# Performance work log

Measured on AMD Instinct MI355X. Metric: run time of the kernel, lower is better.

The kernel has to match this reference:

```python
import jax, jax.numpy as jnp
import numpy as np

B, S, H, W = 256, 512, 1024, 64  # batch, seq, hidden_dim, context_window

def setup_inputs() -> dict:
    key = jax.random.key(0)
    k1, k2, k3, k4, k5, k6 = jax.random.split(key, 6)
    inputs = jax.random.normal(k1, (B, S, H), jnp.float32)
    # lengths must be >= context_window and <= S
    setence_len = W + jax.random.randint(k2, (B,), 0, S - W + 1)
    # parent < W <= len ensures len - parent - 1 >= 0 (valid index)
    parent = jax.random.randint(k3, (B,), 0, W)
    hc = jax.random.normal(k4, (B, H), jnp.float32)
    # nn.Linear(2H, H) params
    W_attn = jax.random.normal(k5, (H, 2 * H), jnp.float32) * (1.0 / np.sqrt(2 * H))
    b_attn = jnp.zeros((H,), jnp.float32)
    # nn.Parameter(torch.rand(H)) -> uniform [0,1)
    v = jax.random.uniform(k6, (H,), jnp.float32)
    return {"inputs": inputs, "hc": hc, "W_attn": W_attn, "b_attn": b_attn,
            "v": v, "setence_len": setence_len, "parent": parent}

def reference(inputs, hc, W_attn, b_attn, v, setence_len, parent):
    # Mt: per-sample window inputs[b, len_b-W:len_b, :] -> [B, W, H]
    idx = setence_len[:, None] - W + jnp.arange(W)[None, :]          # [B, W]
    Mt = jnp.take_along_axis(inputs, idx[:, :, None], axis=1)        # [B, W, H]
    # par: inputs[b, len_b - parent_b - 1, :] -> [B, H]
    pidx = (setence_len - parent - 1)[:, None, None]                 # [B, 1, 1]
    par = jnp.take_along_axis(inputs, pidx, axis=1)[:, 0, :]         # [B, H]
    # h = hc repeated over the window axis -> [B, W, H]
    h = jnp.broadcast_to(hc[:, None, :], Mt.shape)
    # additive (Bahdanau) scoring
    energy = jnp.tanh(jnp.concatenate([h, Mt], axis=-1) @ W_attn.T + b_attn)  # [B, W, H]
    scores = jnp.einsum('h,bwh->bw', v, energy)                      # [B, W]
    attn = jax.nn.softmax(scores, axis=-1)                           # [B, W]
    attn_weights = attn[:, None, :]                                  # [B, 1, W]
    context = jnp.einsum('bw,bwh->bh', attn, Mt)[:, None, :]         # [B, 1, H]
    return attn_weights, context, par
```

## Files before the change

kernel.cpp:

```cpp
#include <hip/hip_runtime.h>
#include <math.h>

#define Bdim 256
#define Sdim 512
#define Hdim 1024
#define Wdim 64
#define BK 32
#define JTILE 256
#define NJT 4
#define MTILE 128
#define KC 4

typedef __attribute__((ext_vector_type(8))) short bf16x8;
typedef __attribute__((ext_vector_type(4))) float f32x4;

#define WS_SCORES_F (NJT * Bdim * Wdim)
#define WS_PART_F   (KC * Bdim * Hdim)
#define WS_WSP_F    (Hdim * Hdim / 2)
#define WS_NEED_BYTES  ((size_t)(WS_SCORES_F + WS_PART_F) * 4)
#define WS_MFMA_BYTES  ((size_t)(WS_SCORES_F + WS_PART_F + WS_WSP_F) * 4)

#define ASTRIDE 140
#define AS_F (BK * ASTRIDE)
#define SMEM_F (AS_F + BK * JTILE)
#define HC0_OFF 0
#define HCW_OFF 2048
#define VS_OFF  2560

__device__ __forceinline__ unsigned pk2(unsigned short a, unsigned short b) {
  return (unsigned)a | ((unsigned)b << 16);
}

__global__ __launch_bounds__(256) void k_wsplit(
    const float* __restrict__ Wa, unsigned short* __restrict__ wsp)
{
  const int j = blockIdx.x;
  const int t = threadIdx.x;
  const float4 xv = *(const float4*)(Wa + (size_t)j * (2 * Hdim) + Hdim + 4 * t);
  unsigned short h[4], l[4];
  #pragma unroll
  for (int e = 0; e < 4; ++e) {
    const float x = ((const float*)&xv)[e];
    const unsigned u = __float_as_uint(x);
    const float hif = __uint_as_float(u & 0xFFFF0000u);
    const float lof = x - hif;
    h[e] = (unsigned short)(u >> 16);
    l[e] = (unsigned short)(__float_as_uint(lof) >> 16);
  }
  const int kc = (4 * t) >> 5, ki = (4 * t) & 31;
  unsigned short* base = wsp + (size_t)j * 2048 + kc * 64 + ki;
  *(ushort4*)(base)      = make_ushort4(h[0], h[1], h[2], h[3]);
  *(ushort4*)(base + 32) = make_ushort4(l[0], l[1], l[2], l[3]);
}

__global__ __launch_bounds__(256) void k_hcw(
    const float* __restrict__ hc, const float* __restrict__ Wa,
    float* __restrict__ part)
{
  const int jt = blockIdx.x, bt = blockIdx.y, kc = blockIdx.z;
  const int t = threadIdx.x;
  const int b0 = bt * 16;
  const int kb = kc * 256;
  __shared__ float As[BK][20];
  __shared__ float Bs[BK][256];
  const int tb = t & 3, tj = t >> 2;
  float acc[4][4] = {{0.f}};
  const float* brow = Wa + (size_t)(jt * 256 + t) * (2 * Hdim) + kb;
  const int r = t & 15, kq = t >> 4;
  for (int k0 = 0; k0 < 256; k0 += BK) {
    float4 bld[8];
    #pragma unroll
    for (int q = 0; q < 8; ++q) bld[q] = *(const float4*)(brow + k0 + q * 4);
    float4 ald = make_float4(0.f, 0.f, 0.f, 0.f);
    if (t < 128) ald = *(const float4*)(hc + (size_t)(b0 + r) * Hdim + kb + k0 + kq * 4);
    __syncthreads();
    #pragma unroll
    for (int q = 0; q < 8; ++q)
      #pragma unroll
      for (int e = 0; e < 4; ++e)
        Bs[q * 4 + e][t] = ((const float*)&bld[q])[e];
    if (t < 128) {
      #pragma unroll
      for (int e = 0; e < 4; ++e) As[kq * 4 + e][r] = ((const float*)&ald)[e];
    }
    __syncthreads();
    #pragma unroll 8
    for (int k = 0; k < BK; ++k) {
      const float4 av = *(const float4*)&As[k][tb * 4];
      const float4 bv = *(const float4*)&Bs[k][tj * 4];
      const float A4[4] = {av.x, av.y, av.z, av.w};
      const float B4[4] = {bv.x, bv.y, bv.z, bv.w};
      #pragma unroll
      for (int i = 0; i < 4; ++i)
        #pragma unroll
        for (int jj = 0; jj < 4; ++jj)
          acc[i][jj] = fmaf(A4[i], B4[jj], acc[i][jj]);
    }
  }
  float* outp = part + (size_t)kc * (Bdim * Hdim);
  #pragma unroll
  for (int i = 0; i < 4; ++i)
    #pragma unroll
    for (int jj = 0; jj < 4; ++jj)
      outp[(size_t)(b0 + tb * 4 + i) * Hdim + jt * 256 + tj * 4 + jj] = acc[i][jj];
}

__global__ __launch_bounds__(512) void k_scores_mfma(
    const float* __restrict__ inputs, const float* __restrict__ ba,
    const float* __restrict__ v, const int* __restrict__ slen,
    float* __restrict__ ws_scores, const float* __restrict__ part,
    const unsigned short* __restrict__ wsp)
{
  const int jt = blockIdx.x;
  const int b0 = blockIdx.y * 4;
  const int t = threadIdx.x;
  const int lane = t & 63, wv = t >> 6, wm = wv >> 1, wn = wv & 1;

  __shared__ uint4 lds4[65536 / 16];
  char* As = (char*)lds4;
  char* Bs = (char*)lds4 + 32768;

  const int ar = t >> 1, ah = t & 1;
  const int ab = ar >> 6;
  const int slA = slen[b0 + ab];
  const float* aptr = inputs +
      ((size_t)(b0 + ab) * Sdim + slA - Wdim + (ar & 63)) * Hdim + ah * 16;
  const int arw = ar & 7;
  char* aw0 = As + ar * 128;
  const int bj = t >> 1, bc = t & 1;
  const unsigned short* bptr = wsp + (size_t)(jt * 256 + bj) * 2048 + bc * 32;
  const int bjw = bj & 7;
  char* bw0 = Bs + bj * 128;

  int aoff[4][2], boff[8][2];
  #pragma unroll
  for (int mt = 0; mt < 4; ++mt) {
    const int row = wm * 64 + mt * 16 + (lane & 15);
    const int s0 = lane >> 4;
    aoff[mt][0] = row * 128 + ((s0 ^ (row & 7)) << 4);
    aoff[mt][1] = row * 128 + (((s0 + 4) ^ (row & 7)) << 4);
  }
  #pragma unroll
  for (int nt = 0; nt < 8; ++nt) {
    const int row = wn * 128 + nt * 16 + (lane & 15);
    const int s0 = lane >> 4;
    boff[nt][0] = row * 128 + ((s0 ^ (row & 7)) << 4);
    boff[nt][1] = row * 128 + (((s0 + 4) ^ (row & 7)) << 4);
  }

  f32x4 acc[4][8];
  #pragma unroll
  for (int mt = 0; mt < 4; ++mt)
    #pragma unroll
    for (int nt = 0; nt < 8; ++nt) {
      f32x4 z = {0.f, 0.f, 0.f, 0.f};
      acc[mt][nt] = z;
    }

  float4 a_ld[4];
  uint4  b_ld[4];
  #pragma unroll
  for (int c = 0; c < 4; ++c) a_ld[c] = *(const float4*)(aptr + c * 4);
  #pragma unroll
  for (int q = 0; q < 4; ++q) b_ld[q] = *(const uint4*)(bptr + q * 8);

  for (int k0 = 0; k0 < Hdim; k0 += 32) {
    __syncthreads();
    unsigned short h[16], l[16];
    #pragma unroll
    for (int c = 0; c < 4; ++c)
      #pragma unroll
      for (int e = 0; e < 4; ++e) {
        const float x = ((const float*)&a_ld[c])[e];
        const unsigned u = __float_as_uint(x);
        const float hif = __uint_as_float(u & 0xFFFF0000u);
        const float lof = x - hif;
        h[c * 4 + e] = (unsigned short)(u >> 16);
        l[c * 4 + e] = (unsigned short)(__float_as_uint(lof) >> 16);
      }
    uint4 H0 = make_uint4(pk2(h[0], h[1]), pk2(h[2], h[3]), pk2(h[4], h[5]), pk2(h[6], h[7]));
    uint4 H1 = make_uint4(pk2(h[8], h[9]), pk2(h[10], h[11]), pk2(h[12], h[13]), pk2(h[14], h[15]));
    uint4 L0 = make_uint4(pk2(l[0], l[1]), pk2(l[2], l[3]), pk2(l[4], l[5]), pk2(l[6], l[7]));
    uint4 L1 = make_uint4(pk2(l[8], l[9]), pk2(l[10], l[11]), pk2(l[12], l[13]), pk2(l[14], l[15]));
    *(uint4*)(aw0 + (((2 * ah + 0) ^ arw) << 4)) = H0;
    *(uint4*)(aw0 + (((2 * ah + 1) ^ arw) << 4)) = H1;
    *(uint4*)(aw0 + (((4 + 2 * ah + 0) ^ arw) << 4)) = L0;
    *(uint4*)(aw0 + (((4 + 2 * ah + 1) ^ arw) << 4)) = L1;
    #pragma unroll
    for (int q = 0; q < 4; ++q)
      *(uint4*)(bw0 + (((bc * 4 + q) ^ bjw) << 4)) = b_ld[q];
    if (k0 + 32 < Hdim) {
      #pragma unroll
      for (int c = 0; c < 4; ++c) a_ld[c] = *(const float4*)(aptr + k0 + 32 + c * 4);
      const int kc = (k0 + 32) >> 5;
      #pragma unroll
      for (int q = 0; q < 4; ++q) b_ld[q] = *(const uint4*)(bptr + kc * 64 + q * 8);
    }
    __syncthreads();
    bf16x8 ahf[4], alf[4];
    #pragma unroll
    for (int mt = 0; mt < 4; ++mt) {
      ahf[mt] = *(const bf16x8*)(As + aoff[mt][0]);
      alf[mt] = *(const bf16x8*)(As + aoff[mt][1]);
    }
    #pragma unroll
    for (int nt = 0; nt < 8; ++nt) {
      const bf16x8 bh = *(const bf16x8*)(Bs + boff[nt][0]);
      const bf16x8 bl = *(const bf16x8*)(Bs + boff[nt][1]);
      #pragma unroll
      for (int mt = 0; mt < 4; ++mt) {
        acc[mt][nt] = __builtin_amdgcn_mfma_f32_16x16x32_bf16(ahf[mt], bh, acc[mt][nt], 0, 0, 0);
        acc[mt][nt] = __builtin_amdgcn_mfma_f32_16x16x32_bf16(alf[mt], bh, acc[mt][nt], 0, 0, 0);
        acc[mt][nt] = __builtin_amdgcn_mfma_f32_16x16x32_bf16(ahf[mt], bl, acc[mt][nt], 0, 0, 0);
      }
    }
  }

  __syncthreads();
  float* scr   = (float*)lds4;
  float* hcw_s = scr;
  float* v_s   = scr + 1024;
  float* red   = scr + 1280;
  for (int idx = t; idx < 1024; idx += 512) {
    const int bb = idx >> 8, jj = idx & 255;
    const int jg = jt * 256 + jj;
    float s = ba[jg];
    #pragma unroll
    for (int kc = 0; kc < KC; ++kc)
      s += part[(size_t)kc * (Bdim * Hdim) + (size_t)(b0 + bb) * Hdim + jg];
    hcw_s[idx] = s;
  }
  if (t < 256) v_s[t] = v[jt * 256 + t];
  __syncthreads();

  float sred[4][4];
  #pragma unroll
  for (int mt = 0; mt < 4; ++mt)
    #pragma unroll
    for (int r = 0; r < 4; ++r) sred[mt][r] = 0.f;
  #pragma unroll
  for (int nt = 0; nt < 8; ++nt) {
    const int col = wn * 128 + nt * 16 + (lane & 15);
    const float hw0 = hcw_s[wm * 256 + col];
    const float vj = v_s[col];
    #pragma unroll
    for (int mt = 0; mt < 4; ++mt)
      #pragma unroll
      for (int r = 0; r < 4; ++r) {
        const float s = ((const float*)&acc[mt][nt])[r] + hw0;
        sred[mt][r] = fmaf(vj, tanhf(s), sred[mt][r]);
      }
  }
  #pragma unroll
  for (int mt = 0; mt < 4; ++mt)
    #pragma unroll
    for (int r = 0; r < 4; ++r) {
      float x = sred[mt][r];
      x += __shfl_xor(x, 1); x += __shfl_xor(x, 2);
      x += __shfl_xor(x, 4); x += __shfl_xor(x, 8);
      sred[mt][r] = x;
    }
  if ((lane & 15) == 0) {
    #pragma unroll
    for (int mt = 0; mt < 4; ++mt)
      #pragma unroll
      for (int r = 0; r < 4; ++r)
        red[wn * 256 + wm * 64 + mt * 16 + (lane >> 4) * 4 + r] = sred[mt][r];
  }
  __syncthreads();
  if (t < 256) {
    const float s = red[t] + red[256 + t];
    ws_scores[(size_t)jt * (Bdim * Wdim) + (size_t)(b0 + (t >> 6)) * Wdim + (t & 63)] = s;
  }
}

template<int USE_PART>
__global__ __launch_bounds__(256, 2) void k_scores(
    const float* __restrict__ inputs, const float* __restrict__ hc,
    const float* __restrict__ Wa, const float* __restrict__ ba,
    const float* __restrict__ v, const int* __restrict__ slen,
    float* __restrict__ ws_scores, const float* __restrict__ part)
{
  const int jt = blockIdx.x;
  const int b0 = blockIdx.y * 2;
  const int t = threadIdx.x;
  __shared__ float smem[SMEM_F];
  float* Bsb = smem + AS_F;

  const int tw = t & 15, tj = t >> 4;
  const int w0 = tw * 8, j0 = tj * 16;
  const int awp = w0 + 4 * (tw >> 2);

  const int ar = t >> 1, ah = t & 1;
  const int absub = ar >> 6;
  const int slA = slen[b0 + absub];
  const float* arow = inputs +
      ((size_t)(b0 + absub) * Sdim + slA - Wdim + (ar & 63)) * Hdim + ah * 16;
  const int aphys = ar + 4 * (ar >> 5);
  const float* brow = Wa + (size_t)(jt * JTILE + t) * (2 * Hdim) + Hdim;

  float acc[8][16];
  #pragma unroll
  for (int i = 0; i < 8; ++i)
    #pragma unroll
    for (int jj = 0; jj < 16; ++jj) acc[i][jj] = 0.f;

  for (int k0 = 0; k0 < Hdim; k0 += BK) {
    float4 a_ld[4];
    #pragma unroll
    for (int c = 0; c < 4; ++c) a_ld[c] = *(const float4*)(arow + k0 + c * 4);
    float4 b_ld[8];
    #pragma unroll
    for (int q = 0; q < 8; ++q) b_ld[q] = *(const float4*)(brow + k0 + q * 4);
    __syncthreads();
    #pragma unroll
    for (int c = 0; c < 4; ++c)
      #pragma unroll
      for (int e = 0; e < 4; ++e)
        smem[(ah * 16 + c * 4 + e) * ASTRIDE + aphys] = ((const float*)&a_ld[c])[e];
    #pragma unroll
    for (int q = 0; q < 8; ++q)
      #pragma unroll
      for (int e = 0; e < 4; ++e)
        Bsb[(q * 4 + e) * JTILE + t] = ((const float*)&b_ld[q])[e];
    __syncthreads();
    #pragma unroll 8
    for (int k = 0; k < BK; ++k) {
      const float* Ak = smem + k * ASTRIDE;
      const float* Bk = Bsb + k * JTILE;
      const float4 av0 = *(const float4*)(Ak + awp);
      const float4 av1 = *(const float4*)(Ak + awp + 4);
      const float4 bv0 = *(const float4*)(Bk + j0);
      const float4 bv1 = *(const float4*)(Bk + j0 + 4);
      const float4 bv2 = *(const float4*)(Bk + j0 + 8);
      const float4 bv3 = *(const float4*)(Bk + j0 + 12);
      const float A8[8]  = {av0.x, av0.y, av0.z, av0.w, av1.x, av1.y, av1.z, av1.w};
      const float B16[16] = {bv0.x, bv0.y, bv0.z, bv0.w, bv1.x, bv1.y, bv1.z, bv1.w,
                             bv2.x, bv2.y, bv2.z, bv2.w, bv3.x, bv3.y, bv3.z, bv3.w};
      #pragma unroll
      for (int wi = 0; wi < 8; ++wi)
        #pragma unroll
        for (int ji = 0; ji < 16; ++ji)
          acc[wi][ji] = fmaf(A8[wi], B16[ji], acc[wi][ji]);
    }
  }

  __syncthreads();
  const int j = jt * JTILE + t;
  if (USE_PART) {
    float h0 = ba[j], h1 = ba[j];
    #pragma unroll
    for (int kc = 0; kc < KC; ++kc) {
      h0 += part[(size_t)kc * (Bdim * Hdim) + (size_t)b0 * Hdim + j];
      h1 += part[(size_t)kc * (Bdim * Hdim) + (size_t)(b0 + 1) * Hdim + j];
    }
    smem[HCW_OFF + t] = h0;
    smem[HCW_OFF + 256 + t] = h1;
    smem[VS_OFF + t] = v[j];
  } else {
    for (int i = t; i < 2 * Hdim; i += 256) smem[HC0_OFF + i] = hc[(size_t)b0 * Hdim + i];
    __syncthreads();
    const float* w1row = Wa + (size_t)j * (2 * Hdim);
    float s0 = 0.f, s1 = 0.f;
    #pragma unroll 4
    for (int k = 0; k < Hdim; k += 4) {
      const float4 wv  = *(const float4*)(w1row + k);
      const float4 h0v = *(const float4*)(smem + HC0_OFF + k);
      const float4 h1v = *(const float4*)(smem + HC0_OFF + Hdim + k);
      s0 = fmaf(wv.x, h0v.x, s0); s0 = fmaf(wv.y, h0v.y, s0);
      s0 = fmaf(wv.z, h0v.z, s0); s0 = fmaf(wv.w, h0v.w, s0);
      s1 = fmaf(wv.x, h1v.x, s1); s1 = fmaf(wv.y, h1v.y, s1);
      s1 = fmaf(wv.z, h1v.z, s1); s1 = fmaf(wv.w, h1v.w, s1);
    }
    __syncthreads();
    smem[HCW_OFF + t] = s0 + ba[j];
    smem[HCW_OFF + 256 + t] = s1 + ba[j];
    smem[VS_OFF + t] = v[j];
  }
  __syncthreads();

  const int bsub = tw >> 3;
  float sloc[8] = {0.f, 0.f, 0.f, 0.f, 0.f, 0.f, 0.f, 0.f};
  #pragma unroll
  for (int ji = 0; ji < 16; ++ji) {
    const float hw = smem[HCW_OFF + bsub * 256 + j0 + ji];
    const float vj = smem[VS_OFF + j0 + ji];
    #pragma unroll
    for (int wi = 0; wi < 8; ++wi)
      sloc[wi] = fmaf(vj, tanhf(acc[wi][ji] + hw), sloc[wi]);
  }
  float* red = smem + AS_F;
  #pragma unroll
  for (int wi = 0; wi < 8; ++wi) red[tj * MTILE + w0 + wi] = sloc[wi];
  __syncthreads();
  if (t < MTILE) {
    float s = 0.f;
    #pragma unroll
    for (int p = 0; p < 16; ++p) s += red[p * MTILE + t];
    ws_scores[(size_t)jt * (Bdim * Wdim) + (size_t)(b0 + (t >> 6)) * Wdim + (t & 63)] = s;
  }
}

__global__ __launch_bounds__(256) void k_finish(
    const float* __restrict__ inputs, const int* __restrict__ slen,
    const int* __restrict__ parent, const float* __restrict__ ws_scores,
    float* __restrict__ out)
{
  const int b = blockIdx.x;
  const int c = blockIdx.y;
  const int t = threadIdx.x;
  const int sl = slen[b];
  __shared__ float attn[64];

  if (t < 64) {
    float s = ws_scores[b * Wdim + t]
            + ws_scores[1 * (Bdim * Wdim) + b * Wdim + t]
            + ws_scores[2 * (Bdim * Wdim) + b * Wdim + t]
            + ws_scores[3 * (Bdim * Wdim) + b * Wdim + t];
    float mx = s;
    #pragma unroll
    for (int off = 32; off > 0; off >>= 1) mx = fmaxf(mx, __shfl_xor(mx, off));
    const float e = __expf(s - mx);
    float sm = e;
    #pragma unroll
    for (int off = 32; off > 0; off >>= 1) sm += __shfl_xor(sm, off);
    const float a = e / sm;
    if (c == 0) out[b * Wdim + t] = a;
    attn[t] = a;
  }
  __syncthreads();

  const float* base = inputs + ((size_t)b * Sdim + sl - Wdim) * Hdim + c * 256;
  float a0 = 0.f;
  #pragma unroll 8
  for (int w = 0; w < Wdim; ++w)
    a0 = fmaf(attn[w], base[(size_t)w * Hdim + t], a0);
  out[Bdim * Wdim + (size_t)b * Hdim + c * 256 + t] = a0;

  const float* pr = inputs + ((size_t)b * Sdim + sl - parent[b] - 1) * Hdim + c * 256;
  out[Bdim * Wdim + Bdim * Hdim + (size_t)b * Hdim + c * 256 + t] = pr[t];
}

extern "C" void kernel_launch(void* const* d_in, const int* in_sizes, int n_in,
                              void* d_out, int out_size, void* d_ws, size_t ws_size,
                              hipStream_t stream) {
  const float* inputs = (const float*)d_in[0];
  const float* hc     = (const float*)d_in[1];
  const float* Wa     = (const float*)d_in[2];
  const float* ba     = (const float*)d_in[3];
  const float* v      = (const float*)d_in[4];
  const int*   slen   = (const int*)d_in[5];
  const int*   parent = (const int*)d_in[6];
  float* out = (float*)d_out;
  float* ws  = (float*)d_ws;
  float* part = ws + WS_SCORES_F;
  unsigned short* wsp = (unsigned short*)(ws + WS_SCORES_F + WS_PART_F);

  if (ws_size >= WS_MFMA_BYTES) {
    k_wsplit<<<dim3(Hdim), 256, 0, stream>>>(Wa, wsp);
    k_hcw<<<dim3(NJT, 16, KC), 256, 0, stream>>>(hc, Wa, part);
    k_scores_mfma<<<dim3(NJT, Bdim / 4), 512, 0, stream>>>(
        inputs, ba, v, slen, ws, part, wsp);
  } else if (ws_size >= WS_NEED_BYTES) {
    k_hcw<<<dim3(NJT, 16, KC), 256, 0, stream>>>(hc, Wa, part);
    k_scores<1><<<dim3(NJT, Bdim / 2), 256, 0, stream>>>(
        inputs, hc, Wa, ba, v, slen, ws, part);
  } else {
    k_scores<0><<<dim3(NJT, Bdim / 2), 256, 0, stream>>>(
        inputs, hc, Wa, ba, v, slen, ws, nullptr);
  }
  k_finish<<<dim3(Bdim, 4), 256, 0, stream>>>(inputs, slen, parent, ws, out);
}
```

Before: 818.2 us.

## Pre-split activations into swizzled bf16 hi/lo and stream via global_load_lds

Adds a prep kernel that gathers each sample's window rows and splits them into bf16 hi/lo pairs. These are stored in global memory already in the swizzled LDS tile layout, and the weight split kernel now writes the same layout. The scores kernel then copies tiles directly into LDS with global_load_lds instead of converting in registers. It also halves the N tile to 128 columns, doubles the grid along N, and raises occupancy via launch bounds. The aim is to remove per-iteration conversion and packing work from the MFMA loop. The costs are a large extra workspace buffer, an extra pass that writes it out, activation data re-read by twice as many N tiles, and an unpipelined load-then-wait per K step.

```diff
diff --git a/kernel.cpp b/kernel.cpp
--- a/kernel.cpp
+++ b/kernel.cpp
@@ -10,15 +10,17 @@
 #define NJT 4
 #define MTILE 128
 #define KC 4
+#define NJT2 8
 
 typedef __attribute__((ext_vector_type(8))) short bf16x8;
 typedef __attribute__((ext_vector_type(4))) float f32x4;
 
-#define WS_SCORES_F (NJT * Bdim * Wdim)
+#define WS_SCORES_F (NJT2 * Bdim * Wdim)
 #define WS_PART_F   (KC * Bdim * Hdim)
 #define WS_WSP_F    (Hdim * Hdim / 2)
-#define WS_NEED_BYTES  ((size_t)(WS_SCORES_F + WS_PART_F) * 4)
-#define WS_MFMA_BYTES  ((size_t)(WS_SCORES_F + WS_PART_F + WS_WSP_F) * 4)
+#define WS_APRE_F   (Bdim * Wdim * Hdim)
+#define WS_NEED_BYTES   ((size_t)(WS_SCORES_F + WS_PART_F) * 4)
+#define WS_MFMA_BYTES   ((size_t)(WS_SCORES_F + WS_PART_F + WS_WSP_F + WS_APRE_F) * 4)
 
 #define ASTRIDE 140
 #define AS_F (BK * ASTRIDE)
@@ -27,8 +29,21 @@
 #define HCW_OFF 2048
 #define VS_OFF  2560
 
-__device__ __forceinline__ unsigned pk2(unsigned short a, unsigned short b) {
-  return (unsigned)a | ((unsigned)b << 16);
+#if defined(__has_builtin)
+#if __has_builtin(__builtin_amdgcn_global_load_lds)
+#define HAS_GLL 1
+#endif
+#endif
+#ifndef HAS_GLL
+#define HAS_GLL 0
+#endif
+
+__device__ __forceinline__ void gll16(const void* g, void* l) {
+#if HAS_GLL
+  __builtin_amdgcn_global_load_lds(
+      (const __attribute__((address_space(1))) void*)g,
+      (__attribute__((address_space(3))) void*)l, 16, 0, 0);
+#endif
 }
 
 __global__ __launch_bounds__(256) void k_wsplit(
@@ -36,6 +51,7 @@
 {
   const int j = blockIdx.x;
   const int t = threadIdx.x;
+  const int jt = j >> 7, jr = j & 127;
   const float4 xv = *(const float4*)(Wa + (size_t)j * (2 * Hdim) + Hdim + 4 * t);
   unsigned short h[4], l[4];
   #pragma unroll
@@ -43,14 +59,42 @@
     const float x = ((const float*)&xv)[e];
     const unsigned u = __float_as_uint(x);
     const float hif = __uint_as_float(u & 0xFFFF0000u);
-    const float lof = x - hif;
     h[e] = (unsigned short)(u >> 16);
-    l[e] = (unsigned short)(__float_as_uint(lof) >> 16);
-  }
-  const int kc = (4 * t) >> 5, ki = (4 * t) & 31;
-  unsigned short* base = wsp + (size_t)j * 2048 + kc * 64 + ki;
-  *(ushort4*)(base)      = make_ushort4(h[0], h[1], h[2], h[3]);
-  *(ushort4*)(base + 32) = make_ushort4(l[0], l[1], l[2], l[3]);
+    l[e] = (unsigned short)(__float_as_uint(x - hif) >> 16);
+  }
+  const int kc = t >> 3;
+  const int ls = (t >> 1) & 3;
+  const int sw = jr & 7;
+  char* base = (char*)wsp + (((size_t)(jt * 32 + kc) * 128 + jr) << 7) + (t & 1) * 8;
+  *(ushort4*)(base + ((ls ^ sw) << 4))       = make_ushort4(h[0], h[1], h[2], h[3]);
+  *(ushort4*)(base + (((ls + 4) ^ sw) << 4)) = make_ushort4(l[0], l[1], l[2], l[3]);
+}
+
+__global__ __launch_bounds__(256) void k_aprep(
+    const float* __restrict__ inputs, const int* __restrict__ slen,
+    unsigned short* __restrict__ apre)
+{
+  const int w = blockIdx.x, b = blockIdx.y;
+  const int t = threadIdx.x;
+  const int gr = b * 64 + w;
+  const int r = gr & 255, bg = gr >> 8;
+  const int sl = slen[b];
+  const float4 xv = *(const float4*)(inputs + ((size_t)b * Sdim + sl - Wdim + w) * Hdim + 4 * t);
+  unsigned short h[4], l[4];
+  #pragma unroll
+  for (int e = 0; e < 4; ++e) {
+    const float x = ((const float*)&xv)[e];
+    const unsigned u = __float_as_uint(x);
+    const float hif = __uint_as_float(u & 0xFFFF0000u);
+    h[e] = (unsigned short)(u >> 16);
+    l[e] = (unsigned short)(__float_as_uint(x - hif) >> 16);
+  }
+  const int kc = t >> 3;
+  const int ls = (t >> 1) & 3;
+  const int sw = r & 7;
+  char* base = (char*)apre + (((size_t)(bg * 32 + kc) * 256 + r) << 7) + (t & 1) * 8;
+  *(ushort4*)(base + ((ls ^ sw) << 4))       = make_ushort4(h[0], h[1], h[2], h[3]);
+  *(ushort4*)(base + (((ls + 4) ^ sw) << 4)) = make_ushort4(l[0], l[1], l[2], l[3]);
 }
 
 __global__ __launch_bounds__(256) void k_hcw(
@@ -105,132 +149,105 @@
       outp[(size_t)(b0 + tb * 4 + i) * Hdim + jt * 256 + tj * 4 + jj] = acc[i][jj];
 }
 
-__global__ __launch_bounds__(512) void k_scores_mfma(
-    const float* __restrict__ inputs, const float* __restrict__ ba,
-    const float* __restrict__ v, const int* __restrict__ slen,
-    float* __restrict__ ws_scores, const float* __restrict__ part,
-    const unsigned short* __restrict__ wsp)
+__global__ __launch_bounds__(512, 4) void k_scores_mfma2(
+    const unsigned short* __restrict__ apre, const unsigned short* __restrict__ wsp,
+    const float* __restrict__ ba, const float* __restrict__ v,
+    float* __restrict__ ws_scores, const float* __restrict__ part)
 {
   const int jt = blockIdx.x;
-  const int b0 = blockIdx.y * 4;
-  const int t = threadIdx.x;
-  const int lane = t & 63, wv = t >> 6, wm = wv >> 1, wn = wv & 1;
-
-  __shared__ uint4 lds4[65536 / 16];
-  char* As = (char*)lds4;
-  char* Bs = (char*)lds4 + 32768;
-
-  const int ar = t >> 1, ah = t & 1;
-  const int ab = ar >> 6;
-  const int slA = slen[b0 + ab];
-  const float* aptr = inputs +
-      ((size_t)(b0 + ab) * Sdim + slA - Wdim + (ar & 63)) * Hdim + ah * 16;
-  const int arw = ar & 7;
-  char* aw0 = As + ar * 128;
-  const int bj = t >> 1, bc = t & 1;
-  const unsigned short* bptr = wsp + (size_t)(jt * 256 + bj) * 2048 + bc * 32;
-  const int bjw = bj & 7;
-  char* bw0 = Bs + bj * 128;
-
-  int aoff[4][2], boff[8][2];
+  const int bg = blockIdx.y;
+  const int t = threadIdx.x;
+  const int lane = t & 63, wv = t >> 6;
+  const int wm = wv >> 1, wn = wv & 1;
+
+  __shared__ uint4 ldsv[49152 / 16];
+  char* lds = (char*)ldsv;
+
+  const int s0 = lane >> 4;
+  int aoff[4][2], boff[4][2];
   #pragma unroll
   for (int mt = 0; mt < 4; ++mt) {
     const int row = wm * 64 + mt * 16 + (lane & 15);
-    const int s0 = lane >> 4;
     aoff[mt][0] = row * 128 + ((s0 ^ (row & 7)) << 4);
     aoff[mt][1] = row * 128 + (((s0 + 4) ^ (row & 7)) << 4);
   }
   #pragma unroll
-  for (int nt = 0; nt < 8; ++nt) {
-    const int row = wn * 128 + nt * 16 + (lane & 15);
-    const int s0 = lane >> 4;
-    boff[nt][0] = row * 128 + ((s0 ^ (row & 7)) << 4);
-    boff[nt][1] = row * 128 + (((s0 + 4) ^ (row & 7)) << 4);
-  }
-
-  f32x4 acc[4][8];
+  for (int nt = 0; nt < 4; ++nt) {
+    const int row = wn * 64 + nt * 16 + (lane & 15);
+    boff[nt][0] = 32768 + row * 128 + ((s0 ^ (row & 7)) << 4);
+    boff[nt][1] = 32768 + row * 128 + (((s0 + 4) ^ (row & 7)) << 4);
+  }
+
+  f32x4 acc[4][4];
   #pragma unroll
   for (int mt = 0; mt < 4; ++mt)
     #pragma unroll
-    for (int nt = 0; nt < 8; ++nt) {
+    for (int nt = 0; nt < 4; ++nt) {
       f32x4 z = {0.f, 0.f, 0.f, 0.f};
       acc[mt][nt] = z;
     }
 
-  float4 a_ld[4];
-  uint4  b_ld[4];
-  #pragma unroll
-  for (int c = 0; c < 4; ++c) a_ld[c] = *(const float4*)(aptr + c * 4);
-  #pragma unroll
-  for (int q = 0; q < 4; ++q) b_ld[q] = *(const uint4*)(bptr + q * 8);
-
-  for (int k0 = 0; k0 < Hdim; k0 += 32) {
-    __syncthreads();
-    unsigned short h[16], l[16];
-    #pragma unroll
-    for (int c = 0; c < 4; ++c)
-      #pragma unroll
-      for (int e = 0; e < 4; ++e) {
-        const float x = ((const float*)&a_ld[c])[e];
-        const unsigned u = __float_as_uint(x);
-        const float hif = __uint_as_float(u & 0xFFFF0000u);
-        const float lof = x - hif;
-        h[c * 4 + e] = (unsigned short)(u >> 16);
-        l[c * 4 + e] = (unsigned short)(__float_as_uint(lof) >> 16);
+  const char* aB = (const char*)apre + ((size_t)bg << 20) + wv * 4096 + (lane << 4);
+  const char* bB = (const char*)wsp + ((size_t)jt << 19) + wv * 2048 + (lane << 4);
+  char* aL = lds + wv * 4096;
+  char* bL = lds + 32768 + wv * 2048;
+
+  for (int kc = 0; kc < 32; ++kc) {
+    __syncthreads();
+    const char* ac = aB + ((size_t)kc << 15);
+    const char* bc = bB + ((size_t)kc << 14);
+#if HAS_GLL
+    gll16(ac,        aL);
+    gll16(ac + 1024, aL + 1024);
+    gll16(ac + 2048, aL + 2048);
+    gll16(ac + 3072, aL + 3072);
+    gll16(bc,        bL);
+    gll16(bc + 1024, bL + 1024);
+    asm volatile("s_waitcnt vmcnt(0)" ::: "memory");
+#else
+    #pragma unroll
+    for (int q = 0; q < 4; ++q)
+      *(uint4*)(aL + q * 1024 + (lane << 4)) = *(const uint4*)(ac + q * 1024);
+    #pragma unroll
+    for (int q = 0; q < 2; ++q)
+      *(uint4*)(bL + q * 1024 + (lane << 4)) = *(const uint4*)(bc + q * 1024);
+#endif
+    __syncthreads();
+
+    bf16x8 bfr[4][2];
+    #pragma unroll
+    for (int nt = 0; nt < 4; ++nt) {
+      bfr[nt][0] = *(const bf16x8*)(lds + boff[nt][0]);
+      bfr[nt][1] = *(const bf16x8*)(lds + boff[nt][1]);
+    }
+    #pragma unroll
+    for (int mt = 0; mt < 4; ++mt) {
+      const bf16x8 ah = *(const bf16x8*)(lds + aoff[mt][0]);
+      const bf16x8 al = *(const bf16x8*)(lds + aoff[mt][1]);
+      #pragma unroll
+      for (int nt = 0; nt < 4; ++nt) {
+        acc[mt][nt] = __builtin_amdgcn_mfma_f32_16x16x32_bf16(ah, bfr[nt][0], acc[mt][nt], 0, 0, 0);
+        acc[mt][nt] = __builtin_amdgcn_mfma_f32_16x16x32_bf16(al, bfr[nt][0], acc[mt][nt], 0, 0, 0);
+        acc[mt][nt] = __builtin_amdgcn_mfma_f32_16x16x32_bf16(ah, bfr[nt][1], acc[mt][nt], 0, 0, 0);
       }
-    uint4 H0 = make_uint4(pk2(h[0], h[1]), pk2(h[2], h[3]), pk2(h[4], h[5]), pk2(h[6], h[7]));
-    uint4 H1 = make_uint4(pk2(h[8], h[9]), pk2(h[10], h[11]), pk2(h[12], h[13]), pk2(h[14], h[15]));
-    uint4 L0 = make_uint4(pk2(l[0], l[1]), pk2(l[2], l[3]), pk2(l[4], l[5]), pk2(l[6], l[7]));
-    uint4 L1 = make_uint4(pk2(l[8], l[9]), pk2(l[10], l[11]), pk2(l[12], l[13]), pk2(l[14], l[15]));
-    *(uint4*)(aw0 + (((2 * ah + 0) ^ arw) << 4)) = H0;
-    *(uint4*)(aw0 + (((2 * ah + 1) ^ arw) << 4)) = H1;
-    *(uint4*)(aw0 + (((4 + 2 * ah + 0) ^ arw) << 4)) = L0;
-    *(uint4*)(aw0 + (((4 + 2 * ah + 1) ^ arw) << 4)) = L1;
-    #pragma unroll
-    for (int q = 0; q < 4; ++q)
-      *(uint4*)(bw0 + (((bc * 4 + q) ^ bjw) << 4)) = b_ld[q];
-    if (k0 + 32 < Hdim) {
-      #pragma unroll
-      for (int c = 0; c < 4; ++c) a_ld[c] = *(const float4*)(aptr + k0 + 32 + c * 4);
-      const int kc = (k0 + 32) >> 5;
-      #pragma unroll
-      for (int q = 0; q < 4; ++q) b_ld[q] = *(const uint4*)(bptr + kc * 64 + q * 8);
-    }
-    __syncthreads();
-    bf16x8 ahf[4], alf[4];
-    #pragma unroll
-    for (int mt = 0; mt < 4; ++mt) {
-      ahf[mt] = *(const bf16x8*)(As + aoff[mt][0]);
-      alf[mt] = *(const bf16x8*)(As + aoff[mt][1]);
-    }
-    #pragma unroll
-    for (int nt = 0; nt < 8; ++nt) {
-      const bf16x8 bh = *(const bf16x8*)(Bs + boff[nt][0]);
-      const bf16x8 bl = *(const bf16x8*)(Bs + boff[nt][1]);
-      #pragma unroll
-      for (int mt = 0; mt < 4; ++mt) {
-        acc[mt][nt] = __builtin_amdgcn_mfma_f32_16x16x32_bf16(ahf[mt], bh, acc[mt][nt], 0, 0, 0);
-        acc[mt][nt] = __builtin_amdgcn_mfma_f32_16x16x32_bf16(alf[mt], bh, acc[mt][nt], 0, 0, 0);
-        acc[mt][nt] = __builtin_amdgcn_mfma_f32_16x16x32_bf16(ahf[mt], bl, acc[mt][nt], 0, 0, 0);
-      }
-    }
-  }
-
-  __syncthreads();
-  float* scr   = (float*)lds4;
-  float* hcw_s = scr;
-  float* v_s   = scr + 1024;
-  float* red   = scr + 1280;
-  for (int idx = t; idx < 1024; idx += 512) {
-    const int bb = idx >> 8, jj = idx & 255;
-    const int jg = jt * 256 + jj;
+    }
+  }
+
+  __syncthreads();
+  float* f = (float*)ldsv;
+  float* hcw_s = f;
+  float* v_s   = f + 512;
+  float* red   = f + 640;
+  {
+    const int bb = t >> 7, jj = t & 127;
+    const int jg = jt * 128 + jj;
     float s = ba[jg];
     #pragma unroll
     for (int kc = 0; kc < KC; ++kc)
-      s += part[(size_t)kc * (Bdim * Hdim) + (size_t)(b0 + bb) * Hdim + jg];
-    hcw_s[idx] = s;
-  }
-  if (t < 256) v_s[t] = v[jt * 256 + t];
+      s += part[(size_t)kc * (Bdim * Hdim) + (size_t)(bg * 4 + bb) * Hdim + jg];
+    hcw_s[t] = s;
+    if (t < 128) v_s[t] = v[jt * 128 + t];
+  }
   __syncthreads();
 
   float sred[4][4];
@@ -239,17 +256,15 @@
     #pragma unroll
     for (int r = 0; r < 4; ++r) sred[mt][r] = 0.f;
   #pragma unroll
-  for (int nt = 0; nt < 8; ++nt) {
-    const int col = wn * 128 + nt * 16 + (lane & 15);
-    const float hw0 = hcw_s[wm * 256 + col];
+  for (int nt = 0; nt < 4; ++nt) {
+    const int col = wn * 64 + nt * 16 + (lane & 15);
+    const float hw = hcw_s[wm * 128 + col];
     const float vj = v_s[col];
     #pragma unroll
     for (int mt = 0; mt < 4; ++mt)
       #pragma unroll
-      for (int r = 0; r < 4; ++r) {
-        const float s = ((const float*)&acc[mt][nt])[r] + hw0;
-        sred[mt][r] = fmaf(vj, tanhf(s), sred[mt][r]);
-      }
+      for (int r = 0; r < 4; ++r)
+        sred[mt][r] = fmaf(vj, tanhf(((const float*)&acc[mt][nt])[r] + hw), sred[mt][r]);
   }
   #pragma unroll
   for (int mt = 0; mt < 4; ++mt)
@@ -270,7 +285,7 @@
   __syncthreads();
   if (t < 256) {
     const float s = red[t] + red[256 + t];
-    ws_scores[(size_t)jt * (Bdim * Wdim) + (size_t)(b0 + (t >> 6)) * Wdim + (t & 63)] = s;
+    ws_scores[(size_t)jt * (Bdim * Wdim) + (size_t)(bg * 4 + (t >> 6)) * Wdim + (t & 63)] = s;
   }
 }
 
@@ -401,6 +416,7 @@
   }
 }
 
+template<int NPART>
 __global__ __launch_bounds__(256) void k_finish(
     const float* __restrict__ inputs, const int* __restrict__ slen,
     const int* __restrict__ parent, const float* __restrict__ ws_scores,
@@ -413,10 +429,10 @@
   __shared__ float attn[64];
 
   if (t < 64) {
-    float s = ws_scores[b * Wdim + t]
-            + ws_scores[1 * (Bdim * Wdim) + b * Wdim + t]
-            + ws_scores[2 * (Bdim * Wdim) + b * Wdim + t]
-            + ws_scores[3 * (Bdim * Wdim) + b * Wdim + t];
+    float s = 0.f;
+    #pragma unroll
+    for (int p = 0; p < NPART; ++p)
+      s += ws_scores[(size_t)p * (Bdim * Wdim) + b * Wdim + t];
     float mx = s;
     #pragma unroll
     for (int off = 32; off > 0; off >>= 1) mx = fmaxf(mx, __shfl_xor(mx, off));
@@ -454,20 +470,24 @@
   float* out = (float*)d_out;
   float* ws  = (float*)d_ws;
   float* part = ws + WS_SCORES_F;
-  unsigned short* wsp = (unsigned short*)(ws + WS_SCORES_F + WS_PART_F);
-
-  if (ws_size >= WS_MFMA_BYTES) {
+  unsigned short* wsp  = (unsigned short*)(ws + WS_SCORES_F + WS_PART_F);
+  unsigned short* apre = (unsigned short*)(ws + WS_SCORES_F + WS_PART_F + WS_WSP_F);
+
+  if (ws_size >= WS_MFMA_BYTES && HAS_GLL) {
     k_wsplit<<<dim3(Hdim), 256, 0, stream>>>(Wa, wsp);
+    k_aprep<<<dim3(Wdim, Bdim), 256, 0, stream>>>(inputs, slen, apre);
     k_hcw<<<dim3(NJT, 16, KC), 256, 0, stream>>>(hc, Wa, part);
-    k_scores_mfma<<<dim3(NJT, Bdim / 4), 512, 0, stream>>>(
-        inputs, ba, v, slen, ws, part, wsp);
+    k_scores_mfma2<<<dim3(NJT2, Bdim / 4), 512, 0, stream>>>(
+        apre, wsp, ba, v, ws, part);
+    k_finish<NJT2><<<dim3(Bdim, 4), 256, 0, stream>>>(inputs, slen, parent, ws, out);
   } else if (ws_size >= WS_NEED_BYTES) {
     k_hcw<<<dim3(NJT, 16, KC), 256, 0, stream>>>(hc, Wa, part);
     k_scores<1><<<dim3(NJT, Bdim / 2), 256, 0, stream>>>(
         inputs, hc, Wa, ba, v, slen, ws, part);
+    k_finish<NJT><<<dim3(Bdim, 4), 256, 0, stream>>>(inputs, slen, parent, ws, out);
   } else {
     k_scores<0><<<dim3(NJT, Bdim / 2), 256, 0, stream>>>(
         inputs, hc, Wa, ba, v, slen, ws, nullptr);
-  }
-  k_finish<<<dim3(Bdim, 4), 256, 0, stream>>>(inputs, slen, parent, ws, out);
-}
+    k_finish<NJT><<<dim3(Bdim, 4), 256, 0, stream>>>(inputs, slen, parent, ws, out);
+  }
+}
```

Measured after the change: 990.4 us. +21.1%, slower.
